# Kernel optimization log

Measured on AMD Instinct MI355X. Metric: run time of the kernel, lower is better.

## Reference

```python
import jax, jax.numpy as jnp
import numpy as np

B, T, E, D = 128, 512, 128, 128

def setup_inputs() -> dict:
    key = jax.random.key(0)
    ks = jax.random.split(key, 20)
    s = 0.05
    return {
        'encoder_states': jax.random.normal(ks[0], (B, T, E), jnp.float32),
        'labels': jax.random.normal(ks[1], (B, T), jnp.float32),
        'init_h': jax.random.normal(ks[2], (B, D), jnp.float32),
        'init_c': jax.random.normal(ks[3], (B, D), jnp.float32),
        'init_ctx': jax.random.normal(ks[4], (B, E), jnp.float32),
        # Attention: W maps concat(h,c) (2D) -> T, U maps E -> T, V maps T -> 1
        'Wa': jax.random.normal(ks[5], (2 * D, T), jnp.float32) * s,
        'ba': jnp.zeros((T,), jnp.float32),
        'Ua': jax.random.normal(ks[6], (E, T), jnp.float32) * s,
        'bu': jnp.zeros((T,), jnp.float32),
        'Va': jax.random.normal(ks[7], (T, 1), jnp.float32) * s,
        'bv': jnp.zeros((1,), jnp.float32),
        # layer_fc_context: (1+E) -> 1
        'Wc': jax.random.normal(ks[8], (1 + E, 1), jnp.float32) * s,
        'bc': jnp.zeros((1,), jnp.float32),
        # LSTMCell: input dim 1, hidden D; gate order i, f, g(candidate), o (Keras)
        'Wk': jax.random.normal(ks[9], (1, 4 * D), jnp.float32) * s,
        'Wr': jax.random.normal(ks[10], (D, 4 * D), jnp.float32) * s,
        'bl': jnp.zeros((4 * D,), jnp.float32),
        # prediction FCs: (D+E)->D, D->1
        'W1': jax.random.normal(ks[11], (D + E, D), jnp.float32) * s,
        'b1': jnp.zeros((D,), jnp.float32),
        'W2': jax.random.normal(ks[12], (D, 1), jnp.float32) * s,
        'b2': jnp.zeros((1,), jnp.float32),
    }


def reference(encoder_states, labels, init_h, init_c, init_ctx,
              Wa, ba, Ua, bu, Va, bv, Wc, bc, Wk, Wr, bl, W1, b1, W2, b2):
    # Loop-invariant attention term U(encoder_states): (B, T, T)
    u_enc = jnp.einsum('bte,tn->btn'[0:14].replace('t','t') if False else 'bte,en->btn', encoder_states, Ua) + bu

    def step(carry, label_t):
        h, c, _ctx = carry
        # additive attention over time axis
        s = jnp.concatenate([h, c], axis=-1) @ Wa + ba            # (B, T)
        e = jnp.tanh(u_enc + s[:, None, :])                        # (B, T, T)
        score = (e @ Va)[..., 0] + bv                              # (B, T)
        w = jax.nn.softmax(score, axis=1)                          # (B, T)
        ctx = jnp.einsum('bt,bte->be', w, encoder_states)          # (B, E)
        # context-gated input
        y = jnp.concatenate([label_t[:, None], ctx], axis=-1) @ Wc + bc   # (B, 1)
        # Keras LSTMCell step
        z = y @ Wk + h @ Wr + bl                                   # (B, 4D)
        i, f, g, o = jnp.split(z, 4, axis=-1)
        c_new = jax.nn.sigmoid(f) * c + jax.nn.sigmoid(i) * jnp.tanh(g)
        h_new = jax.nn.sigmoid(o) * jnp.tanh(c_new)
        return (h_new, c_new, ctx), None

    (h, c, ctx), _ = jax.lax.scan(step, (init_h, init_c, init_ctx), labels.T)
    pred = (jnp.concatenate([h, ctx], axis=-1) @ W1 + b1) @ W2 + b2   # (B, 1)
    return pred
```

## Files before the change

kernel.cpp:

```cpp
#include <hip/hip_runtime.h>
#include <hip/hip_fp16.h>

#define B_ 128
#define T_ 512
#define E_ 128
#define D_ 128

#define C2f 2.885390081777927f
#define L2E 1.4426950408889634f

__device__ __forceinline__ float rcpf_(float x){ return __builtin_amdgcn_rcpf(x); }
__device__ __forceinline__ float ex2_(float x){ return __builtin_amdgcn_exp2f(x); }

__device__ __forceinline__ void gstoref(float* p, float v){
    __hip_atomic_store(p, v, __ATOMIC_RELAXED, __HIP_MEMORY_SCOPE_AGENT);
}
__device__ __forceinline__ float gloadf(const float* p){
    return __hip_atomic_load(p, __ATOMIC_RELAXED, __HIP_MEMORY_SCOPE_AGENT);
}
__device__ __forceinline__ void flag_set(int* p, int v){
    __hip_atomic_store(p, v, __ATOMIC_RELEASE, __HIP_MEMORY_SCOPE_AGENT);
}
__device__ __forceinline__ void flag_wait(int* p, int v){
    int it = 0;
    while (__hip_atomic_load(p, __ATOMIC_ACQUIRE, __HIP_MEMORY_SCOPE_AGENT) < v
           && it < (1 << 26)){ it++; __builtin_amdgcn_s_sleep(2); }
}

__global__ __launch_bounds__(256) void transpose_half(const float* __restrict__ in,
                                                      __half* __restrict__ out,
                                                      int K, int N){
    __shared__ float tile[32][33];
    int n0 = blockIdx.x * 32, k0 = blockIdx.y * 32;
    int tx = threadIdx.x & 31, ty = threadIdx.x >> 5;
    #pragma unroll
    for (int i = ty; i < 32; i += 8)
        tile[i][tx] = in[(size_t)(k0 + i) * N + n0 + tx];
    __syncthreads();
    #pragma unroll
    for (int i = ty; i < 32; i += 8)
        out[(size_t)(n0 + i) * K + k0 + tx] = __float2half(tile[tx][i]);
}

__global__ __launch_bounds__(512) void g_kernel(const float* __restrict__ enc,
                                                const float* __restrict__ Wc,
                                                float* __restrict__ g){
    int b = blockIdx.x, t = threadIdx.x;
    const float4* ep = (const float4*)(enc + ((size_t)b * T_ + t) * E_);
    float acc = 0.f;
    #pragma unroll
    for (int i = 0; i < 32; i++){
        float4 ev = ep[i];
        acc = fmaf(ev.x, Wc[1 + 4*i + 0], acc);
        acc = fmaf(ev.y, Wc[1 + 4*i + 1], acc);
        acc = fmaf(ev.z, Wc[1 + 4*i + 2], acc);
        acc = fmaf(ev.w, Wc[1 + 4*i + 3], acc);
    }
    g[(size_t)b * T_ + t] = acc;
}

__global__ __launch_bounds__(256) void uenc_kernel(const float* __restrict__ enc,
                                                   const float* __restrict__ Ua,
                                                   const float* __restrict__ bu,
                                                   __half* __restrict__ P){
    int b = blockIdx.z;
    int t0 = blockIdx.x * 64;
    int n0 = blockIdx.y * 64;
    int tt = threadIdx.x & 63;
    int ng = threadIdx.x >> 6;
    const float* erow = enc + ((size_t)b * T_ + (t0 + tt)) * E_;
    const float* uap  = Ua + n0 + ng * 16;
    float acc[16];
    #pragma unroll
    for (int i = 0; i < 16; i++) acc[i] = 0.f;
    #pragma unroll 2
    for (int e0 = 0; e0 < E_; e0 += 4){
        float4 av = *(const float4*)(erow + e0);
        #pragma unroll
        for (int ee = 0; ee < 4; ee++){
            float a = (ee==0)?av.x:(ee==1)?av.y:(ee==2)?av.z:av.w;
            const float4* u4 = (const float4*)(uap + (size_t)(e0+ee) * T_);
            float4 x0 = u4[0], x1 = u4[1], x2 = u4[2], x3 = u4[3];
            acc[0]  = fmaf(a, x0.x, acc[0]);  acc[1]  = fmaf(a, x0.y, acc[1]);
            acc[2]  = fmaf(a, x0.z, acc[2]);  acc[3]  = fmaf(a, x0.w, acc[3]);
            acc[4]  = fmaf(a, x1.x, acc[4]);  acc[5]  = fmaf(a, x1.y, acc[5]);
            acc[6]  = fmaf(a, x1.z, acc[6]);  acc[7]  = fmaf(a, x1.w, acc[7]);
            acc[8]  = fmaf(a, x2.x, acc[8]);  acc[9]  = fmaf(a, x2.y, acc[9]);
            acc[10] = fmaf(a, x2.z, acc[10]); acc[11] = fmaf(a, x2.w, acc[11]);
            acc[12] = fmaf(a, x3.x, acc[12]); acc[13] = fmaf(a, x3.y, acc[13]);
            acc[14] = fmaf(a, x3.z, acc[14]); acc[15] = fmaf(a, x3.w, acc[15]);
        }
    }
    int nb = n0 + ng * 16;
    #pragma unroll
    for (int i = 0; i < 16; i++){
        float u = acc[i] + bu[nb + i];
        P[(size_t)b * T_ * T_ + (size_t)(nb + i) * T_ + t0 + tt] = __float2half(ex2_(C2f * u));
    }
}

__device__ __forceinline__ void dot8(float& acc, uint4 wv, float4 ha, float4 hb){
    float2 f0 = __half22float2(*reinterpret_cast<__half2*>(&wv.x));
    float2 f1 = __half22float2(*reinterpret_cast<__half2*>(&wv.y));
    float2 f2 = __half22float2(*reinterpret_cast<__half2*>(&wv.z));
    float2 f3 = __half22float2(*reinterpret_cast<__half2*>(&wv.w));
    acc = fmaf(ha.x, f0.x, acc); acc = fmaf(ha.y, f0.y, acc);
    acc = fmaf(ha.z, f1.x, acc); acc = fmaf(ha.w, f1.y, acc);
    acc = fmaf(hb.x, f2.x, acc); acc = fmaf(hb.y, f2.y, acc);
    acc = fmaf(hb.z, f3.x, acc); acc = fmaf(hb.w, f3.y, acc);
}

__device__ __forceinline__ void acc8(uint4 pv, float2 qv,
    float& a0, float& a1, float& a2, float& a3,
    float& a4, float& a5, float& a6, float& a7)
{
    float2 f0 = __half22float2(*reinterpret_cast<__half2*>(&pv.x));
    float2 f1 = __half22float2(*reinterpret_cast<__half2*>(&pv.y));
    float2 f2 = __half22float2(*reinterpret_cast<__half2*>(&pv.z));
    float2 f3 = __half22float2(*reinterpret_cast<__half2*>(&pv.w));
    float m;
    m = fmaf(f0.x, qv.x, 1.f); a0 = fmaf(rcpf_(m), qv.y, a0);
    m = fmaf(f0.y, qv.x, 1.f); a1 = fmaf(rcpf_(m), qv.y, a1);
    m = fmaf(f1.x, qv.x, 1.f); a2 = fmaf(rcpf_(m), qv.y, a2);
    m = fmaf(f1.y, qv.x, 1.f); a3 = fmaf(rcpf_(m), qv.y, a3);
    m = fmaf(f2.x, qv.x, 1.f); a4 = fmaf(rcpf_(m), qv.y, a4);
    m = fmaf(f2.y, qv.x, 1.f); a5 = fmaf(rcpf_(m), qv.y, a5);
    m = fmaf(f3.x, qv.x, 1.f); a6 = fmaf(rcpf_(m), qv.y, a6);
    m = fmaf(f3.y, qv.x, 1.f); a7 = fmaf(rcpf_(m), qv.y, a7);
}

__global__ __launch_bounds__(1024) void decoder_kernel(
    const float* __restrict__ enc,
    const float* __restrict__ labels,
    const float* __restrict__ init_h, const float* __restrict__ init_c,
    const float* __restrict__ Va,
    const float* __restrict__ ba, const float* __restrict__ bl,
    const float* __restrict__ Wc, const float* __restrict__ bc,
    const float* __restrict__ Wk,
    const float* __restrict__ W1, const float* __restrict__ b1,
    const float* __restrict__ W2, const float* __restrict__ b2,
    const __half* __restrict__ Wa_t, const __half* __restrict__ Wr_t,
    const __half* __restrict__ Pw, const float* __restrict__ gbuf,
    float* __restrict__ psbuf,
    int* __restrict__ fA, int* __restrict__ fB,
    float* __restrict__ out)
{
    __shared__ __align__(16) __half Plds[128 * 512];
    __shared__ __align__(16) float hc_s[256];
    __shared__ __align__(16) float ctx_s[128];
    __shared__ __align__(16) float Q_s[256];
    __shared__ __align__(16) float Vam_s[256];
    __shared__ __align__(16) float sc[512];
    __shared__ __align__(16) float rz_s[512];
    __shared__ __align__(16) float g_s[512];
    __shared__ __align__(16) float scratch[4096];
    __shared__ __align__(16) float ba_s[256], bl_s[256];
    __shared__ __align__(16) float Wk_s[512];
    __shared__ float Wc_s[132];
    __shared__ float red[20];

    const int tid = threadIdx.x;
    const int b = blockIdx.x;
    const int h_ = blockIdx.y;
    const int par_stride = B_ * 2;

    if (tid < 128){
        hc_s[tid]       = init_h[b*128 + tid];
        hc_s[128 + tid] = init_c[b*128 + tid];
    }
    if (tid < 256){
        Vam_s[tid] = -2.f * Va[256*h_ + tid];
        ba_s[tid]  = ba[256*h_ + tid];
        bl_s[tid]  = bl[256*h_ + tid];
    }
    if (tid < 512){
        Wk_s[tid] = Wk[tid];
        g_s[tid]  = gbuf[(size_t)b * T_ + tid];
    }
    if (tid < 129) Wc_s[tid] = Wc[tid];
    if (tid == 129) Wc_s[130] = bc[0];

    const __half* Pb  = Pw + ((size_t)b * T_ + 256 * h_) * T_;
    const uint4*  Pb4 = (const uint4*)Pb;

    {
        int wid = tid >> 6, lane = tid & 63;
        for (int r = wid; r < 128; r += 16){
            int g = r >> 3, j = r & 7;
            *((uint4*)Plds + (size_t)r * 64 + lane) =
                Pb4[(size_t)(16*g + j) * 64 + lane];
        }
    }
    __syncthreads();

    int* myfA = &fA[b*2 + h_];   int* pfA = &fA[b*2 + (1 - h_)];
    int* myfB = &fB[b*2 + h_];   int* pfB = &fB[b*2 + (1 - h_)];

    const int np_ = tid & 255;
    const int kq_ = tid >> 8;

    for (int t = 0; t < T_; t++){
        const int par = t & 1;
        float* psme = psbuf + ((size_t)par * par_stride + b*2 + h_)     * 768;
        float* pspr = psbuf + ((size_t)par * par_stride + b*2 + (1-h_)) * 768;

        {
            const float4* hc4 = (const float4*)hc_s;
            {
                float acc = (kq_ == 0) ? ba_s[np_] : 0.f;
                const uint4* wa = (const uint4*)(Wa_t + (size_t)(256*h_ + np_) * 256 + kq_ * 64);
                #pragma unroll 4
                for (int i = 0; i < 8; i++){
                    uint4 wv = wa[i];
                    dot8(acc, wv, hc4[kq_*16 + 2*i], hc4[kq_*16 + 2*i + 1]);
                }
                scratch[kq_*256 + np_] = acc;
            }
            {
                float accr = (kq_ == 0) ? bl_s[np_] : 0.f;
                const uint4* wr = (const uint4*)(Wr_t + (size_t)(256*h_ + np_) * 128 + kq_ * 32);
                #pragma unroll
                for (int i = 0; i < 4; i++){
                    uint4 wv = wr[i];
                    dot8(accr, wv, hc4[kq_*8 + 2*i], hc4[kq_*8 + 2*i + 1]);
                }
                scratch[1024 + kq_*256 + np_] = accr;
            }
        }
        __syncthreads();
        if (tid < 256){
            float s = scratch[tid] + scratch[256+tid] + scratch[512+tid] + scratch[768+tid];
            Q_s[tid] = ex2_(C2f * s);
        } else if (tid < 512){
            int m = tid - 256;
            float rzv = scratch[1024+m] + scratch[1280+m] + scratch[1536+m] + scratch[1792+m];
            rz_s[256*h_ + m] = rzv;
            gstoref(&psme[512 + m], rzv);
        }
        __syncthreads();

        float a0=0.f,a1=0.f,a2=0.f,a3=0.f,a4=0.f,a5=0.f,a6=0.f,a7=0.f;
        {
            int q = tid & 63, g = tid >> 6;
            const uint4* Pl = (const uint4*)Plds + (size_t)(8*g) * 64 + q;
            #pragma unroll
            for (int j = 0; j < 8; j++){
                uint4 pv = Pl[j * 64];
                float2 qv = make_float2(Q_s[16*g + j], Vam_s[16*g + j]);
                acc8(pv, qv, a0,a1,a2,a3,a4,a5,a6,a7);
            }
            const uint4* Pg = Pb4 + (size_t)(16*g + 8) * 64 + q;
            #pragma unroll 4
            for (int j = 0; j < 8; j++){
                uint4 pv = Pg[(size_t)j * 64];
                float2 qv = make_float2(Q_s[16*g + 8 + j], Vam_s[16*g + 8 + j]);
                acc8(pv, qv, a0,a1,a2,a3,a4,a5,a6,a7);
            }
        }
        {
            int q = tid & 63, g = tid >> 6;
            float4* o = (float4*)(scratch + (g & 7)*512 + q*8);
            if (g >= 8){
                o[0] = make_float4(a0,a1,a2,a3);
                o[1] = make_float4(a4,a5,a6,a7);
            }
            __syncthreads();
            if (g < 8){
                float4 p0 = o[0], p1 = o[1];
                o[0] = make_float4(a0+p0.x, a1+p0.y, a2+p0.z, a3+p0.w);
                o[1] = make_float4(a4+p1.x, a5+p1.y, a6+p1.z, a7+p1.w);
            }
        }
        __syncthreads();
        if (tid < 512){
            float v = 0.f;
            #pragma unroll
            for (int g = 0; g < 8; g++) v += scratch[g*512 + tid];
            sc[tid] = v;
            gstoref(&psme[tid], v);
        }
        __syncthreads();
        if (tid == 0){ flag_set(myfA, t + 1); flag_wait(pfA, t + 1); }
        __syncthreads();
        if (tid < 512){
            float score = sc[tid] + gloadf(&pspr[tid]);
            float p = ex2_(score * L2E);
            sc[tid] = p;
            float ss = p;
            float sg = p * g_s[tid];
            #pragma unroll
            for (int off = 32; off; off >>= 1){
                ss += __shfl_xor(ss, off);
                sg += __shfl_xor(sg, off);
            }
            if ((tid & 63) == 0){ red[tid >> 6] = ss; red[8 + (tid >> 6)] = sg; }
        } else if (tid < 768){
            int m = tid - 512;
            rz_s[256*(1-h_) + m] = gloadf(&pspr[512 + m]);
        }
        __syncthreads();
        if (tid == 0){ flag_set(myfB, t + 1); flag_wait(pfB, t + 1); }
        __syncthreads();

        if (tid < 128){
            float dn = red[0]+red[1]+red[2]+red[3]+red[4]+red[5]+red[6]+red[7];
            float pg = red[8]+red[9]+red[10]+red[11]+red[12]+red[13]+red[14]+red[15];
            float lab = labels[(size_t)b * T_ + t];
            float y = fmaf(lab, Wc_s[0], pg * rcpf_(dn) + Wc_s[130]);
            float zi = rz_s[tid]       + y * Wk_s[tid];
            float zf = rz_s[128 + tid] + y * Wk_s[128 + tid];
            float zg = rz_s[256 + tid] + y * Wk_s[256 + tid];
            float zo = rz_s[384 + tid] + y * Wk_s[384 + tid];
            float si = rcpf_(1.f + ex2_(-L2E * zi));
            float sf = rcpf_(1.f + ex2_(-L2E * zf));
            float so = rcpf_(1.f + ex2_(-L2E * zo));
            float tg_ = 1.f - 2.f * rcpf_(ex2_(C2f * zg) + 1.f);
            float cn = sf * hc_s[128 + tid] + si * tg_;
            float tc = 1.f - 2.f * rcpf_(ex2_(C2f * cn) + 1.f);
            hc_s[128 + tid] = cn;
            hc_s[tid] = so * tc;
        }
        __syncthreads();
    }

    {
        int eq = tid & 31, tg = tid >> 5;
        float4 acc = make_float4(0.f,0.f,0.f,0.f);
        const float4* ep = (const float4*)(enc + ((size_t)b*T_ + tg*16)*E_) + eq;
        #pragma unroll
        for (int i = 0; i < 16; i++){
            float w = sc[tg*16 + i];
            float4 ev = ep[(size_t)i * 32];
            acc.x = fmaf(w, ev.x, acc.x); acc.y = fmaf(w, ev.y, acc.y);
            acc.z = fmaf(w, ev.z, acc.z); acc.w = fmaf(w, ev.w, acc.w);
        }
        *(float4*)(scratch + tg*128 + eq*4) = acc;
    }
    __syncthreads();
    if (tid < 128){
        float s = 0.f;
        #pragma unroll
        for (int g2 = 0; g2 < 32; g2++) s += scratch[g2*128 + tid];
        float dn = red[0]+red[1]+red[2]+red[3]+red[4]+red[5]+red[6]+red[7];
        ctx_s[tid] = s * rcpf_(dn);
    }
    __syncthreads();

    if (tid < 128){
        float acc = b1[tid];
        for (int k = 0; k < 128; k++) acc = fmaf(hc_s[k],  W1[k*128 + tid], acc);
        for (int k = 0; k < 128; k++) acc = fmaf(ctx_s[k], W1[(128+k)*128 + tid], acc);
        scratch[tid] = acc * W2[tid];
    }
    __syncthreads();
    if (h_ == 0 && tid < 64){
        float a = scratch[tid] + scratch[64 + tid];
        #pragma unroll
        for (int off = 32; off; off >>= 1) a += __shfl_xor(a, off);
        if (tid == 0) out[b] = a + b2[0];
    }
}

extern "C" void kernel_launch(void* const* d_in, const int* in_sizes, int n_in,
                              void* d_out, int out_size, void* d_ws, size_t ws_size,
                              hipStream_t stream){
    const float* enc      = (const float*)d_in[0];
    const float* labels   = (const float*)d_in[1];
    const float* init_h   = (const float*)d_in[2];
    const float* init_c   = (const float*)d_in[3];
    const float* Wa = (const float*)d_in[5];
    const float* ba = (const float*)d_in[6];
    const float* Ua = (const float*)d_in[7];
    const float* bu = (const float*)d_in[8];
    const float* Va = (const float*)d_in[9];
    const float* Wc = (const float*)d_in[11];
    const float* bc = (const float*)d_in[12];
    const float* Wk = (const float*)d_in[13];
    const float* Wr = (const float*)d_in[14];
    const float* bl = (const float*)d_in[15];
    const float* W1 = (const float*)d_in[16];
    const float* b1 = (const float*)d_in[17];
    const float* W2 = (const float*)d_in[18];
    const float* b2 = (const float*)d_in[19];

    char* ws = (char*)d_ws;
    const size_t szP = (size_t)B_ * T_ * T_ * 2;
    const size_t szWa = 512 * 256 * 2;
    const size_t szWr = 512 * 128 * 2;
    const size_t szG  = (size_t)B_ * T_ * 4;

    __half* P    = (__half*)ws;
    __half* Wa_t = (__half*)(ws + szP);
    __half* Wr_t = (__half*)(ws + szP + szWa);
    float*  gbuf = (float*)(ws + szP + szWa + szWr);
    float* psbuf = (float*)(ws + szP + szWa + szWr + szG);
    int*   flags = (int*)(psbuf + 2*256*768);
    int* fA = flags;
    int* fB = flags + 256;

    hipMemsetAsync(flags, 0, 512 * sizeof(int), stream);

    transpose_half<<<dim3(16, 8, 1), 256, 0, stream>>>(Wa, Wa_t, 256, 512);
    transpose_half<<<dim3(16, 4, 1), 256, 0, stream>>>(Wr, Wr_t, 128, 512);
    g_kernel<<<B_, 512, 0, stream>>>(enc, Wc, gbuf);

    dim3 g1(T_/64, T_/64, B_);
    uenc_kernel<<<g1, 256, 0, stream>>>(enc, Ua, bu, P);

    decoder_kernel<<<dim3(B_, 2), 1024, 0, stream>>>(enc,
        labels, init_h, init_c, Va, ba, bl, Wc, bc, Wk, W1, b1, W2, b2,
        Wa_t, Wr_t, P, gbuf, psbuf, fA, fB, (float*)d_out);
}
```

Before: 9.113 ms.

## Replace LDS scratch reductions with LDS atomics and cache more P rows

Frees the 16KB scratch buffer by replacing the staged partial-sum reductions (gate/attention projections and score accumulation) with LDS float atomicAdd into small accumulators, dropping one barrier. The freed shared memory is used to cache 143 of the 256 P rows in LDS instead of 128, so fewer P rows are streamed from global memory each step. The costs are contention on LDS atomics, a data-dependent loop split that limits unrolling, and a change in floating-point summation order.

```diff
diff --git a/kernel.cpp b/kernel.cpp
--- a/kernel.cpp
+++ b/kernel.cpp
@@ -5,12 +5,17 @@
 #define T_ 512
 #define E_ 128
 #define D_ 128
+#define RLDS 143
 
 #define C2f 2.885390081777927f
 #define L2E 1.4426950408889634f
 
 __device__ __forceinline__ float rcpf_(float x){ return __builtin_amdgcn_rcpf(x); }
 __device__ __forceinline__ float ex2_(float x){ return __builtin_amdgcn_exp2f(x); }
+
+__device__ __forceinline__ void lds_fadd(float* p, float v){
+    atomicAdd(p, v);
+}
 
 __device__ __forceinline__ void gstoref(float* p, float v){
     __hip_atomic_store(p, v, __ATOMIC_RELAXED, __HIP_MEMORY_SCOPE_AGENT);
@@ -145,7 +150,7 @@
     int* __restrict__ fA, int* __restrict__ fB,
     float* __restrict__ out)
 {
-    __shared__ __align__(16) __half Plds[128 * 512];
+    __shared__ __align__(16) char pool_[RLDS * 1024];
     __shared__ __align__(16) float hc_s[256];
     __shared__ __align__(16) float ctx_s[128];
     __shared__ __align__(16) float Q_s[256];
@@ -153,8 +158,9 @@
     __shared__ __align__(16) float sc[512];
     __shared__ __align__(16) float rz_s[512];
     __shared__ __align__(16) float g_s[512];
-    __shared__ __align__(16) float scratch[4096];
-    __shared__ __align__(16) float ba_s[256], bl_s[256];
+    __shared__ __align__(16) float spre[256];
+    __shared__ __align__(16) float rzpre[256];
+    __shared__ __align__(16) float scoreacc[8 * 65];
     __shared__ __align__(16) float Wk_s[512];
     __shared__ float Wc_s[132];
     __shared__ float red[20];
@@ -164,32 +170,36 @@
     const int h_ = blockIdx.y;
     const int par_stride = B_ * 2;
 
+    float ba_reg = 0.f, bl_reg = 0.f;
+
     if (tid < 128){
         hc_s[tid]       = init_h[b*128 + tid];
         hc_s[128 + tid] = init_c[b*128 + tid];
     }
     if (tid < 256){
         Vam_s[tid] = -2.f * Va[256*h_ + tid];
-        ba_s[tid]  = ba[256*h_ + tid];
-        bl_s[tid]  = bl[256*h_ + tid];
+        ba_reg = ba[256*h_ + tid];
+        spre[tid] = ba_reg;
+    } else if (tid < 512){
+        bl_reg = bl[256*h_ + tid - 256];
+        rzpre[tid - 256] = bl_reg;
     }
     if (tid < 512){
         Wk_s[tid] = Wk[tid];
         g_s[tid]  = gbuf[(size_t)b * T_ + tid];
     }
+    if (tid < 520) scoreacc[tid] = 0.f;
     if (tid < 129) Wc_s[tid] = Wc[tid];
     if (tid == 129) Wc_s[130] = bc[0];
 
     const __half* Pb  = Pw + ((size_t)b * T_ + 256 * h_) * T_;
     const uint4*  Pb4 = (const uint4*)Pb;
+    uint4* Plds4 = (uint4*)pool_;
 
     {
         int wid = tid >> 6, lane = tid & 63;
-        for (int r = wid; r < 128; r += 16){
-            int g = r >> 3, j = r & 7;
-            *((uint4*)Plds + (size_t)r * 64 + lane) =
-                Pb4[(size_t)(16*g + j) * 64 + lane];
-        }
+        for (int r = wid; r < RLDS; r += 16)
+            Plds4[r * 64 + lane] = Pb4[(size_t)r * 64 + lane];
     }
     __syncthreads();
 
@@ -206,76 +216,73 @@
 
         {
             const float4* hc4 = (const float4*)hc_s;
+            float acc = 0.f, accr = 0.f;
             {
-                float acc = (kq_ == 0) ? ba_s[np_] : 0.f;
                 const uint4* wa = (const uint4*)(Wa_t + (size_t)(256*h_ + np_) * 256 + kq_ * 64);
                 #pragma unroll 4
                 for (int i = 0; i < 8; i++){
                     uint4 wv = wa[i];
                     dot8(acc, wv, hc4[kq_*16 + 2*i], hc4[kq_*16 + 2*i + 1]);
                 }
-                scratch[kq_*256 + np_] = acc;
             }
             {
-                float accr = (kq_ == 0) ? bl_s[np_] : 0.f;
                 const uint4* wr = (const uint4*)(Wr_t + (size_t)(256*h_ + np_) * 128 + kq_ * 32);
                 #pragma unroll
                 for (int i = 0; i < 4; i++){
                     uint4 wv = wr[i];
                     dot8(accr, wv, hc4[kq_*8 + 2*i], hc4[kq_*8 + 2*i + 1]);
                 }
-                scratch[1024 + kq_*256 + np_] = accr;
             }
+            lds_fadd(&spre[np_], acc);
+            lds_fadd(&rzpre[np_], accr);
         }
         __syncthreads();
         if (tid < 256){
-            float s = scratch[tid] + scratch[256+tid] + scratch[512+tid] + scratch[768+tid];
+            float s = spre[tid];
+            spre[tid] = ba_reg;
             Q_s[tid] = ex2_(C2f * s);
         } else if (tid < 512){
             int m = tid - 256;
-            float rzv = scratch[1024+m] + scratch[1280+m] + scratch[1536+m] + scratch[1792+m];
+            float rzv = rzpre[m];
+            rzpre[m] = bl_reg;
             rz_s[256*h_ + m] = rzv;
             gstoref(&psme[512 + m], rzv);
         }
         __syncthreads();
 
-        float a0=0.f,a1=0.f,a2=0.f,a3=0.f,a4=0.f,a5=0.f,a6=0.f,a7=0.f;
         {
             int q = tid & 63, g = tid >> 6;
-            const uint4* Pl = (const uint4*)Plds + (size_t)(8*g) * 64 + q;
-            #pragma unroll
-            for (int j = 0; j < 8; j++){
+            int base = 16 * g;
+            int nl = RLDS - base; nl = nl < 0 ? 0 : (nl > 16 ? 16 : nl);
+            float a0=0.f,a1=0.f,a2=0.f,a3=0.f,a4=0.f,a5=0.f,a6=0.f,a7=0.f;
+            const uint4* Pl = Plds4 + (size_t)base * 64 + q;
+            #pragma unroll 4
+            for (int j = 0; j < nl; j++){
                 uint4 pv = Pl[j * 64];
-                float2 qv = make_float2(Q_s[16*g + j], Vam_s[16*g + j]);
+                float2 qv = make_float2(Q_s[base + j], Vam_s[base + j]);
                 acc8(pv, qv, a0,a1,a2,a3,a4,a5,a6,a7);
             }
-            const uint4* Pg = Pb4 + (size_t)(16*g + 8) * 64 + q;
+            const uint4* Pg = Pb4 + (size_t)base * 64 + q;
             #pragma unroll 4
-            for (int j = 0; j < 8; j++){
+            for (int j = nl; j < 16; j++){
                 uint4 pv = Pg[(size_t)j * 64];
-                float2 qv = make_float2(Q_s[16*g + 8 + j], Vam_s[16*g + 8 + j]);
+                float2 qv = make_float2(Q_s[base + j], Vam_s[base + j]);
                 acc8(pv, qv, a0,a1,a2,a3,a4,a5,a6,a7);
             }
-        }
-        {
-            int q = tid & 63, g = tid >> 6;
-            float4* o = (float4*)(scratch + (g & 7)*512 + q*8);
-            if (g >= 8){
-                o[0] = make_float4(a0,a1,a2,a3);
-                o[1] = make_float4(a4,a5,a6,a7);
-            }
-            __syncthreads();
-            if (g < 8){
-                float4 p0 = o[0], p1 = o[1];
-                o[0] = make_float4(a0+p0.x, a1+p0.y, a2+p0.z, a3+p0.w);
-                o[1] = make_float4(a4+p1.x, a5+p1.y, a6+p1.z, a7+p1.w);
-            }
+            lds_fadd(&scoreacc[0*65 + q], a0);
+            lds_fadd(&scoreacc[1*65 + q], a1);
+            lds_fadd(&scoreacc[2*65 + q], a2);
+            lds_fadd(&scoreacc[3*65 + q], a3);
+            lds_fadd(&scoreacc[4*65 + q], a4);
+            lds_fadd(&scoreacc[5*65 + q], a5);
+            lds_fadd(&scoreacc[6*65 + q], a6);
+            lds_fadd(&scoreacc[7*65 + q], a7);
         }
         __syncthreads();
         if (tid < 512){
-            float v = 0.f;
-            #pragma unroll
-            for (int g = 0; g < 8; g++) v += scratch[g*512 + tid];
+            int qq = tid >> 3, kk = tid & 7;
+            float v = scoreacc[kk*65 + qq];
+            scoreacc[kk*65 + qq] = 0.f;
             sc[tid] = v;
             gstoref(&psme[tid], v);
         }
@@ -323,6 +330,7 @@
         __syncthreads();
     }
 
+    float* escr = (float*)pool_;
     {
         int eq = tid & 31, tg = tid >> 5;
         float4 acc = make_float4(0.f,0.f,0.f,0.f);
@@ -334,13 +342,13 @@
             acc.x = fmaf(w, ev.x, acc.x); acc.y = fmaf(w, ev.y, acc.y);
             acc.z = fmaf(w, ev.z, acc.z); acc.w = fmaf(w, ev.w, acc.w);
         }
-        *(float4*)(scratch + tg*128 + eq*4) = acc;
+        *(float4*)(escr + tg*128 + eq*4) = acc;
     }
     __syncthreads();
     if (tid < 128){
         float s = 0.f;
         #pragma unroll
-        for (int g2 = 0; g2 < 32; g2++) s += scratch[g2*128 + tid];
+        for (int g2 = 0; g2 < 32; g2++) s += escr[g2*128 + tid];
         float dn = red[0]+red[1]+red[2]+red[3]+red[4]+red[5]+red[6]+red[7];
         ctx_s[tid] = s * rcpf_(dn);
     }
@@ -350,11 +358,11 @@
         float acc = b1[tid];
         for (int k = 0; k < 128; k++) acc = fmaf(hc_s[k],  W1[k*128 + tid], acc);
         for (int k = 0; k < 128; k++) acc = fmaf(ctx_s[k], W1[(128+k)*128 + tid], acc);
-        scratch[tid] = acc * W2[tid];
+        escr[tid] = acc * W2[tid];
     }
     __syncthreads();
     if (h_ == 0 && tid < 64){
-        float a = scratch[tid] + scratch[64 + tid];
+        float a = escr[tid] + escr[64 + tid];
         #pragma unroll
         for (int off = 32; off; off >>= 1) a += __shfl_xor(a, off);
         if (tid == 0) out[b] = a + b2[0];
```

Result: slower. 15.64 ms (+71.6%).
